# Optimization experiments

Hardware: AMD Instinct MI355X
Metric: run time of the kernel (lower is better)

The kernel has to match this reference:

```python
import jax, jax.numpy as jnp
import numpy as np

B, S, H, F = 4, 2048, 1024, 4096
E, K = 8, 2


def setup_inputs() -> dict:
    key = jax.random.key(0)
    ks = jax.random.split(key, 8)
    s1 = 1.0 / np.sqrt(H)
    s2 = 1.0 / np.sqrt(F)
    return {
        "hidden_states": jax.random.normal(ks[0], (B, S, H), dtype=jnp.float32),
        "w1": jax.random.normal(ks[1], (E, H, F), dtype=jnp.float32) * s1,
        "b1": jnp.zeros((E, F), dtype=jnp.float32),
        "w2": jax.random.normal(ks[2], (E, F, H), dtype=jnp.float32) * s2,
        "b2": jnp.zeros((E, H), dtype=jnp.float32),
        "router_w": jax.random.normal(ks[3], (H, E), dtype=jnp.float32) * s1,
        "router_b": jnp.zeros((E,), dtype=jnp.float32),
    }


def reference(hidden_states, w1, b1, w2, b2, router_w, router_b):
    b, s, h = hidden_states.shape
    x = hidden_states.reshape(-1, h)              # [T, H]
    # --- router: softmax over expert logits, top-k, renormalize ---
    logits = x @ router_w + router_b              # [T, E]
    probs = jax.nn.softmax(logits, axis=-1)
    top_w, top_i = jax.lax.top_k(probs, K)        # [T, K]
    top_w = top_w / jnp.sum(top_w, axis=-1, keepdims=True)
    # --- dispatch/combine: per-expert FFN, weighted sum (same math as
    # gather/scatter loop in the torch module, expressed densely per expert) ---
    out = jnp.zeros_like(x)
    for e in range(E):
        we = jnp.sum(jnp.where(top_i == e, top_w, 0.0), axis=-1)   # [T]
        he = jax.nn.gelu(x @ w1[e] + b1[e]) @ w2[e] + b2[e]        # [T, H]
        out = out + we[:, None] * he
    return out.reshape(b, s, h)
```

## Files before the change

### kernel.cpp

```cpp
#include <hip/hip_runtime.h>
#include <cstdint>
#include <cstddef>

#define T_TOK 8192
#define HD 1024
#define FD 4096
#define NE 8
#define RCAP 17408

typedef __bf16 bf16_t;
typedef __bf16 bf16x8 __attribute__((ext_vector_type(8)));
typedef __bf16 bf16x4 __attribute__((ext_vector_type(4)));
typedef float floatx4 __attribute__((ext_vector_type(4)));

#define BM 128
#define BN 128
#define BK 64

__device__ __forceinline__ float gelu_tanh(float x) {
    float x3 = x * x * x;
    float t = tanhf(0.7978845608028654f * (x + 0.044715f * x3));
    return 0.5f * x * (1.0f + t);
}

__device__ __forceinline__ void stage16(const bf16_t* g, bf16_t* lds_base) {
    __builtin_amdgcn_global_load_lds(
        (const __attribute__((address_space(1))) void*)g,
        (__attribute__((address_space(3))) void*)lds_base,
        16, 0, 0);
}

__global__ __launch_bounds__(256) void transpose_conv_kernel(
    const float* __restrict__ in, bf16_t* __restrict__ out, int R, int C)
{
    __shared__ float tile[64][65];
    const int e = blockIdx.z;
    const int c0 = blockIdx.x * 64;
    const int r0 = blockIdx.y * 64;
    const float* src = in + (size_t)e * R * C;
    bf16_t* dst = out + (size_t)e * R * C;

    const int tc = (threadIdx.x & 15) * 4;
    const int tr = threadIdx.x >> 4;
    #pragma unroll
    for (int p = 0; p < 4; ++p) {
        int r = tr + p * 16;
        float4 v = *(const float4*)(src + (size_t)(r0 + r) * C + c0 + tc);
        tile[r][tc]     = v.x;
        tile[r][tc + 1] = v.y;
        tile[r][tc + 2] = v.z;
        tile[r][tc + 3] = v.w;
    }
    __syncthreads();
    const int rw = (threadIdx.x & 15) * 4;
    const int cw = threadIdx.x >> 4;
    #pragma unroll
    for (int p = 0; p < 4; ++p) {
        int c = cw + p * 16;
        bf16x4 o;
        o[0] = (bf16_t)tile[rw][c];
        o[1] = (bf16_t)tile[rw + 1][c];
        o[2] = (bf16_t)tile[rw + 2][c];
        o[3] = (bf16_t)tile[rw + 3][c];
        *(bf16x4*)(dst + (size_t)(c0 + c) * R + r0 + rw) = o;
    }
}

__global__ __launch_bounds__(256) void router_kernel(
    const float* __restrict__ x, const float* __restrict__ rw,
    const float* __restrict__ rb,
    int* __restrict__ tok_e, float* __restrict__ tok_w, int* __restrict__ counts)
{
    const int t = blockIdx.x * 4 + (threadIdx.x >> 6);
    const int lane = threadIdx.x & 63;
    const float* xr = x + (size_t)t * HD;
    float acc[NE];
    #pragma unroll
    for (int e = 0; e < NE; ++e) acc[e] = 0.f;
    #pragma unroll 4
    for (int i = 0; i < HD / 64; ++i) {
        int h = lane + 64 * i;
        float xv = xr[h];
        const float4* w4 = (const float4*)(rw + (size_t)h * NE);
        float4 wa = w4[0], wb = w4[1];
        acc[0] += xv * wa.x; acc[1] += xv * wa.y;
        acc[2] += xv * wa.z; acc[3] += xv * wa.w;
        acc[4] += xv * wb.x; acc[5] += xv * wb.y;
        acc[6] += xv * wb.z; acc[7] += xv * wb.w;
    }
    #pragma unroll
    for (int s = 32; s > 0; s >>= 1)
        #pragma unroll
        for (int e = 0; e < NE; ++e)
            acc[e] += __shfl_xor(acc[e], s, 64);
    if (lane == 0) {
        float l[NE];
        #pragma unroll
        for (int e = 0; e < NE; ++e) l[e] = acc[e] + rb[e];
        int e1 = 0;
        #pragma unroll
        for (int e = 1; e < NE; ++e) if (l[e] > l[e1]) e1 = e;
        int e2 = (e1 == 0) ? 1 : 0;
        #pragma unroll
        for (int e = 0; e < NE; ++e) {
            if (e == e1 || e == e2) continue;
            if (l[e] > l[e2]) e2 = e;
        }
        float m = l[e1];
        float q1 = 1.0f;
        float q2 = expf(l[e2] - m);
        float inv = 1.0f / (q1 + q2);
        tok_e[t * 2]     = e1;
        tok_e[t * 2 + 1] = e2;
        tok_w[t * 2]     = q1 * inv;
        tok_w[t * 2 + 1] = q2 * inv;
        atomicAdd(&counts[e1], 1);
        atomicAdd(&counts[e2], 1);
    }
}

__global__ void offsets_kernel(const int* __restrict__ counts,
                               int* __restrict__ offsets, int* __restrict__ cursors)
{
    if (threadIdx.x == 0) {
        int cum = 0;
        for (int e = 0; e < NE; ++e) {
            offsets[e] = cum;
            cursors[e] = cum;
            cum += (counts[e] + BM - 1) & ~(BM - 1);
        }
    }
}

__global__ __launch_bounds__(256) void gather_kernel(
    const float* __restrict__ x, const int* __restrict__ tok_e,
    const float* __restrict__ tok_w, int* __restrict__ cursors,
    bf16_t* __restrict__ Xg, int* __restrict__ rows_token, float* __restrict__ rows_w)
{
    const int pair = blockIdx.x * 4 + (threadIdx.x >> 6);
    const int lane = threadIdx.x & 63;
    const int t = pair >> 1;
    int pos;
    if (lane == 0) {
        int e = tok_e[pair];
        pos = atomicAdd(&cursors[e], 1);
        rows_token[pos] = t;
        rows_w[pos] = tok_w[pair];
    }
    pos = __shfl(pos, 0, 64);
    const float4* src = (const float4*)(x + (size_t)t * HD);
    bf16_t* dst = Xg + (size_t)pos * HD;
    #pragma unroll
    for (int i = 0; i < HD / 256; ++i) {
        float4 v = src[lane + 64 * i];
        int base = (lane + 64 * i) * 4;
        bf16x4 o;
        o[0] = (bf16_t)v.x; o[1] = (bf16_t)v.y;
        o[2] = (bf16_t)v.z; o[3] = (bf16_t)v.w;
        *(bf16x4*)(dst + base) = o;
    }
}

template<int KDIM>
__device__ __forceinline__ void gemm_tile(
    const bf16_t* __restrict__ aG,
    const bf16_t* __restrict__ bG,
    bf16_t* __restrict__ As, bf16_t* __restrict__ Bs,
    floatx4 acc[4][4])
{
    const int tid = threadIdx.x;
    const int lane = tid & 63;
    const int wave = tid >> 6;
    const int quad = lane >> 4;
    const int l16 = lane & 15;
    const int wm = (wave & 1) * 64;
    const int wn = (wave >> 1) * 64;
    const int srow = lane >> 3;
    const int scol = ((lane & 7) ^ srow) << 3;
    const int wrow = wave * 32;

    for (int k0 = 0; k0 < KDIM; k0 += BK) {
        #pragma unroll
        for (int p = 0; p < 4; ++p) {
            int r = wrow + p * 8;
            stage16(aG + (size_t)(r + srow) * KDIM + k0 + scol, As + r * BK);
            stage16(bG + (size_t)(r + srow) * KDIM + k0 + scol, Bs + r * BK);
        }
        __syncthreads();
        #pragma unroll
        for (int kk = 0; kk < BK; kk += 32) {
            bf16x8 af[4], bfr[4];
            #pragma unroll
            for (int i = 0; i < 4; ++i) {
                int row = wm + i * 16 + l16;
                int slot = ((kk >> 3) + quad) ^ (row & 7);
                af[i] = *(const bf16x8*)(As + row * BK + (slot << 3));
            }
            #pragma unroll
            for (int i = 0; i < 4; ++i) {
                int row = wn + i * 16 + l16;
                int slot = ((kk >> 3) + quad) ^ (row & 7);
                bfr[i] = *(const bf16x8*)(Bs + row * BK + (slot << 3));
            }
            #pragma unroll
            for (int i = 0; i < 4; ++i)
                #pragma unroll
                for (int j = 0; j < 4; ++j)
                    acc[i][j] = __builtin_amdgcn_mfma_f32_16x16x32_bf16(
                        af[i], bfr[j], acc[i][j], 0, 0, 0);
        }
        __syncthreads();
    }
}

__device__ __forceinline__ int xcd_swizzle(int bid, int nwg) {
    int cpx = nwg >> 3;
    return (bid & 7) * cpx + (bid >> 3);
}

__global__ __launch_bounds__(256) void ffn1_kernel(
    const bf16_t* __restrict__ Xg, const bf16_t* __restrict__ w1t,
    const float* __restrict__ b1, bf16_t* __restrict__ Hb,
    const int* __restrict__ counts, const int* __restrict__ offsets)
{
    const int nwg = (FD / BN) * (T_TOK / BM) * NE;
    int wg = xcd_swizzle(blockIdx.x, nwg);
    const int nt = wg & (FD / BN - 1);
    int rem = wg >> 5;
    const int mtile = rem & (T_TOK / BM - 1);
    const int e = rem >> 6;

    const int cnt = counts[e];
    if (mtile * BM >= cnt) return;
    const int m_base = offsets[e] + mtile * BM;
    const int n_base = nt * BN;

    __shared__ bf16_t As[BM * BK];
    __shared__ bf16_t Bs[BN * BK];
    floatx4 acc[4][4] = {};

    gemm_tile<HD>(Xg + (size_t)m_base * HD,
                  w1t + ((size_t)e * FD + n_base) * HD, As, Bs, acc);

    const int lane = threadIdx.x & 63;
    const int wave = threadIdx.x >> 6;
    const int quad = lane >> 4;
    const int l16 = lane & 15;
    const int wm = (wave & 1) * 64;
    const int wn = (wave >> 1) * 64;
    #pragma unroll
    for (int i = 0; i < 4; ++i) {
        int rl = wm + i * 16 + quad * 4;
        #pragma unroll
        for (int j = 0; j < 4; ++j) {
            int col = n_base + wn + j * 16 + l16;
            float bias = b1[e * FD + col];
            #pragma unroll
            for (int r = 0; r < 4; ++r) {
                float v = acc[i][j][r] + bias;
                Hb[(size_t)(m_base + rl + r) * FD + col] = (bf16_t)gelu_tanh(v);
            }
        }
    }
}

__global__ __launch_bounds__(256) void ffn2_kernel(
    const bf16_t* __restrict__ Hb, const bf16_t* __restrict__ w2t,
    const float* __restrict__ b2, float* __restrict__ out,
    const int* __restrict__ counts, const int* __restrict__ offsets,
    const int* __restrict__ rows_token, const float* __restrict__ rows_w)
{
    const int nwg = (HD / BN) * (T_TOK / BM) * NE;
    int wg = xcd_swizzle(blockIdx.x, nwg);
    const int nt = wg & (HD / BN - 1);
    int rem = wg >> 3;
    const int mtile = rem & (T_TOK / BM - 1);
    const int e = rem >> 6;

    const int cnt = counts[e];
    if (mtile * BM >= cnt) return;
    const int m_base = offsets[e] + mtile * BM;
    const int n_base = nt * BN;

    __shared__ bf16_t As[BM * BK];
    __shared__ bf16_t Bs[BN * BK];
    floatx4 acc[4][4] = {};

    gemm_tile<FD>(Hb + (size_t)m_base * FD,
                  w2t + ((size_t)e * HD + n_base) * FD, As, Bs, acc);

    const int lane = threadIdx.x & 63;
    const int wave = threadIdx.x >> 6;
    const int quad = lane >> 4;
    const int l16 = lane & 15;
    const int wm = (wave & 1) * 64;
    const int wn = (wave >> 1) * 64;
    const int loc_base = mtile * BM;
    #pragma unroll
    for (int i = 0; i < 4; ++i) {
        int rl = wm + i * 16 + quad * 4;
        #pragma unroll
        for (int j = 0; j < 4; ++j) {
            int col = n_base + wn + j * 16 + l16;
            float bias = b2[e * HD + col];
            #pragma unroll
            for (int r = 0; r < 4; ++r) {
                if (loc_base + rl + r < cnt) {
                    int gr = m_base + rl + r;
                    int token = rows_token[gr];
                    float wgt = rows_w[gr];
                    float v = acc[i][j][r] + bias;
                    atomicAdd(&out[(size_t)token * HD + col], wgt * v);
                }
            }
        }
    }
}

extern "C" void kernel_launch(void* const* d_in, const int* in_sizes, int n_in,
                              void* d_out, int out_size, void* d_ws, size_t ws_size,
                              hipStream_t stream)
{
    (void)in_sizes; (void)n_in; (void)ws_size;
    const float* x  = (const float*)d_in[0];
    const float* w1 = (const float*)d_in[1];
    const float* b1 = (const float*)d_in[2];
    const float* w2 = (const float*)d_in[3];
    const float* b2 = (const float*)d_in[4];
    const float* rw = (const float*)d_in[5];
    const float* rb = (const float*)d_in[6];
    float* out = (float*)d_out;

    char* ws = (char*)d_ws;
    size_t off = 0;
    auto alloc = [&](size_t bytes) -> void* {
        void* p = ws + off;
        off = (off + bytes + 255) & ~(size_t)255;
        return p;
    };
    int*    counts     = (int*)alloc(NE * sizeof(int));
    int*    cursors    = (int*)alloc(NE * sizeof(int));
    int*    offsets    = (int*)alloc(NE * sizeof(int));
    int*    tok_e      = (int*)alloc((size_t)T_TOK * 2 * sizeof(int));
    float*  tok_w      = (float*)alloc((size_t)T_TOK * 2 * sizeof(float));
    int*    rows_token = (int*)alloc((size_t)RCAP * sizeof(int));
    float*  rows_w     = (float*)alloc((size_t)RCAP * sizeof(float));
    bf16_t* Xg         = (bf16_t*)alloc((size_t)RCAP * HD * sizeof(bf16_t));
    bf16_t* Hb         = (bf16_t*)alloc((size_t)RCAP * FD * sizeof(bf16_t));
    bf16_t* w1t        = (bf16_t*)alloc((size_t)NE * FD * HD * sizeof(bf16_t));
    bf16_t* w2t        = (bf16_t*)alloc((size_t)NE * HD * FD * sizeof(bf16_t));

    hipMemsetAsync(counts, 0, NE * sizeof(int), stream);
    hipMemsetAsync(out, 0, (size_t)out_size * sizeof(float), stream);

    transpose_conv_kernel<<<dim3(FD / 64, HD / 64, NE), 256, 0, stream>>>(w1, w1t, HD, FD);
    transpose_conv_kernel<<<dim3(HD / 64, FD / 64, NE), 256, 0, stream>>>(w2, w2t, FD, HD);

    router_kernel<<<dim3(T_TOK / 4), 256, 0, stream>>>(x, rw, rb, tok_e, tok_w, counts);

    offsets_kernel<<<dim3(1), 64, 0, stream>>>(counts, offsets, cursors);

    gather_kernel<<<dim3(T_TOK * 2 / 4), 256, 0, stream>>>(
        x, tok_e, tok_w, cursors, Xg, rows_token, rows_w);

    ffn1_kernel<<<dim3((FD / BN) * (T_TOK / BM) * NE), 256, 0, stream>>>(
        Xg, w1t, b1, Hb, counts, offsets);

    ffn2_kernel<<<dim3((HD / BN) * (T_TOK / BM) * NE), 256, 0, stream>>>(
        Hb, w2t, b2, out, counts, offsets, rows_token, rows_w);
}
```

Before: 1.332 ms.

## Double-buffer LDS tiles to overlap global loads with MFMA compute

Doubles the shared-memory A/B tile buffers in the shared GEMM tile routine and prefetches the next K-slice while the current one is computed. It uses explicit vmcnt waits and s_barriers in place of the two __syncthreads per iteration. The aim is to hide global-to-LDS latency behind the matrix cores in both FFN kernels. LDS use per block doubles to 64KB, which may reduce occupancy. The vmcnt(8) count assumes stage16 issues exactly one load per call.

```diff
diff --git a/kernel.cpp b/kernel.cpp
--- a/kernel.cpp
+++ b/kernel.cpp
@@ -165,7 +165,8 @@
 __device__ __forceinline__ void gemm_tile(
     const bf16_t* __restrict__ aG,
     const bf16_t* __restrict__ bG,
-    bf16_t* __restrict__ As, bf16_t* __restrict__ Bs,
+    bf16_t* __restrict__ As,
+    bf16_t* __restrict__ Bs,
     floatx4 acc[4][4])
 {
     const int tid = threadIdx.x;
@@ -179,14 +180,23 @@
     const int scol = ((lane & 7) ^ srow) << 3;
     const int wrow = wave * 32;
 
-    for (int k0 = 0; k0 < KDIM; k0 += BK) {
+    constexpr int NT = KDIM / BK;
+
+    auto STAGE = [&](int buf, int t) {
+        bf16_t* as = As + buf * (BM * BK);
+        bf16_t* bs = Bs + buf * (BM * BK);
+        const size_t kofs = (size_t)t * BK;
         #pragma unroll
         for (int p = 0; p < 4; ++p) {
             int r = wrow + p * 8;
-            stage16(aG + (size_t)(r + srow) * KDIM + k0 + scol, As + r * BK);
-            stage16(bG + (size_t)(r + srow) * KDIM + k0 + scol, Bs + r * BK);
-        }
-        __syncthreads();
+            stage16(aG + (size_t)(r + srow) * KDIM + kofs + scol, as + r * BK);
+            stage16(bG + (size_t)(r + srow) * KDIM + kofs + scol, bs + r * BK);
+        }
+    };
+
+    auto COMPUTE = [&](int buf) {
+        const bf16_t* as = As + buf * (BM * BK);
+        const bf16_t* bs = Bs + buf * (BM * BK);
         #pragma unroll
         for (int kk = 0; kk < BK; kk += 32) {
             bf16x8 af[4], bfr[4];
@@ -194,13 +204,13 @@
             for (int i = 0; i < 4; ++i) {
                 int row = wm + i * 16 + l16;
                 int slot = ((kk >> 3) + quad) ^ (row & 7);
-                af[i] = *(const bf16x8*)(As + row * BK + (slot << 3));
+                af[i] = *(const bf16x8*)(as + row * BK + (slot << 3));
             }
             #pragma unroll
             for (int i = 0; i < 4; ++i) {
                 int row = wn + i * 16 + l16;
                 int slot = ((kk >> 3) + quad) ^ (row & 7);
-                bfr[i] = *(const bf16x8*)(Bs + row * BK + (slot << 3));
+                bfr[i] = *(const bf16x8*)(bs + row * BK + (slot << 3));
             }
             #pragma unroll
             for (int i = 0; i < 4; ++i)
@@ -209,8 +219,21 @@
                     acc[i][j] = __builtin_amdgcn_mfma_f32_16x16x32_bf16(
                         af[i], bfr[j], acc[i][j], 0, 0, 0);
         }
-        __syncthreads();
-    }
+    };
+
+    STAGE(0, 0);
+    for (int t = 0; t < NT - 1; ++t) {
+        STAGE((t + 1) & 1, t + 1);
+        asm volatile("s_waitcnt vmcnt(8)" ::: "memory");
+        __builtin_amdgcn_sched_barrier(0);
+        __builtin_amdgcn_s_barrier();
+        COMPUTE(t & 1);
+        __builtin_amdgcn_s_barrier();
+    }
+    asm volatile("s_waitcnt vmcnt(0)" ::: "memory");
+    __builtin_amdgcn_sched_barrier(0);
+    __builtin_amdgcn_s_barrier();
+    COMPUTE((NT - 1) & 1);
 }
 
 __device__ __forceinline__ int xcd_swizzle(int bid, int nwg) {
@@ -235,8 +258,8 @@
     const int m_base = offsets[e] + mtile * BM;
     const int n_base = nt * BN;
 
-    __shared__ bf16_t As[BM * BK];
-    __shared__ bf16_t Bs[BN * BK];
+    __shared__ bf16_t As[2 * BM * BK];
+    __shared__ bf16_t Bs[2 * BN * BK];
     floatx4 acc[4][4] = {};
 
     gemm_tile<HD>(Xg + (size_t)m_base * HD,
@@ -282,8 +305,8 @@
     const int m_base = offsets[e] + mtile * BM;
     const int n_base = nt * BN;
 
-    __shared__ bf16_t As[BM * BK];
-    __shared__ bf16_t Bs[BN * BK];
+    __shared__ bf16_t As[2 * BM * BK];
+    __shared__ bf16_t Bs[2 * BN * BK];
     floatx4 acc[4][4] = {};
 
     gemm_tile<FD>(Hb + (size_t)m_base * FD,
```

After: 1.286 ms. -3.5%, faster.
